# Kernel tuning notes

Measured on AMD Instinct MI355X. Metric: run time of the kernel, lower is better.

The kernel has to match this reference:

```python
import jax, jax.numpy as jnp
import numpy as np

# ReRAM crossbar constants (from init_kwargs)
GMAX = 0.000333
GMIN = 3.33e-07
DELTA_G = GMAX - GMIN
VDD = 3.3
N_LVL_V = 256
DELTA_V = VDD / (N_LVL_V - 1)
CRXB_COL, CRXB_ROW, CRXB_SIZE = 16, 16, 64
BATCH = 4096


def setup_inputs() -> dict:
    key = jax.random.key(0)
    k1, k2 = jax.random.split(key)
    inputs = jax.random.normal(k1, (BATCH, 1, CRXB_ROW, CRXB_SIZE, 1), dtype=jnp.float32)
    weight = jax.random.normal(k2, (CRXB_COL, CRXB_ROW, CRXB_SIZE, CRXB_SIZE), dtype=jnp.float32)
    nchout_index = jnp.arange(CRXB_COL * CRXB_SIZE, dtype=jnp.int64)
    return {"inputs": inputs, "weight": weight, "nchout_index": nchout_index}


def reference(inputs, weight, nchout_index):
    # DAC: scale digital input to voltage
    input_crxb = inputs * DELTA_V                      # [N,1,row,S,1]
    # w2g: map signed weight to positive/negative conductance crossbars
    g_pos = GMIN + jax.nn.relu(weight) * DELTA_G       # [col,row,S,S]
    g_neg = GMIN + jax.nn.relu(-weight) * DELTA_G
    # split pos/neg crossbar matmuls (broadcast over batch), fused subtract
    out = jnp.matmul(g_pos, input_crxb) - jnp.matmul(g_neg, input_crxb)  # [N,col,row,S,1]
    out = jnp.swapaxes(out, 2, 3)                      # [N,col,S,row,1]
    n = out.shape[0]
    out = out.reshape(n, CRXB_COL * CRXB_SIZE, CRXB_ROW, 1)
    out = jnp.take(out, nchout_index, axis=1)          # output channel select
    return jnp.squeeze(out, axis=-1)                   # [N, col*S, row]
```

## Files before the change

### kernel.cpp

```cpp
#include <hip/hip_runtime.h>
#include <hip/hip_bf16.h>
#include <stdint.h>


using bf16x8 = __attribute__((ext_vector_type(8))) short;
using f32x4  = __attribute__((ext_vector_type(4))) float;

#define NPT 16
#define NIT 16
#define PITCH_B 2064
#define BUFB 33024
#define LDS_BYTES (2*BUFB)

__device__ inline ushort f2bf(float f) {
  uint32_t u = __builtin_bit_cast(uint32_t, f);
  u += 0x7FFFu + ((u >> 16) & 1u);
  return (ushort)(u >> 16);
}

__device__ inline bf16x8 cvt8v(float4 a, float4 b) {
  union { bf16x8 v; ushort u[8]; } r;
  r.u[0] = f2bf(a.x); r.u[1] = f2bf(a.y); r.u[2] = f2bf(a.z); r.u[3] = f2bf(a.w);
  r.u[4] = f2bf(b.x); r.u[5] = f2bf(b.y); r.u[6] = f2bf(b.z); r.u[7] = f2bf(b.w);
  return r.v;
}

__global__ __launch_bounds__(512, 4)
void crxb_kernel(const float* __restrict__ X, const float* __restrict__ W,
                 float* __restrict__ out) {
  extern __shared__ char smem[];
  const int t   = threadIdx.x;
  const int bid = blockIdx.x;
  const int ngrp = ((bid & 7) << 1) | ((bid >> 3) & 1);
  const int mt   = bid >> 4;
  const int c  = mt >> 1;
  const int i0 = (mt & 1) << 5;
  const int m0 = mt << 5;

  const int wid = t >> 6;
  const int l   = t & 63;
  const int lr  = l & 15;
  const int lk  = l >> 4;
  const int r0w = wid << 1;

  bf16x8 A[2][2][2];
  #pragma unroll
  for (int rr = 0; rr < 2; ++rr)
    #pragma unroll
    for (int ks = 0; ks < 2; ++ks)
      #pragma unroll
      for (int a = 0; a < 2; ++a) {
        const float* gw = W + (((size_t)(c * 16 + r0w + rr) * 64) + (i0 + a * 16 + lr)) * 64
                            + ks * 32 + lk * 8;
        A[rr][ks][a] = cvt8v(*(const float4*)gw, *(const float4*)(gw + 4));
      }

  const float S = (float)((0.000333 - 3.33e-07) * (3.3 / 255.0));

  {
    #pragma unroll
    for (int p = 0; p < 4; ++p) {
      int u = p * 512 + t;
      int n = u >> 7, r = (u >> 3) & 15, k8 = u & 7;
      const float* gx = X + (((size_t)(ngrp * 256 + n) * 16) + r) * 64 + k8 * 8;
      *(bf16x8*)(smem + (size_t)n * PITCH_B + r * 128 + k8 * 16) =
          cvt8v(*(const float4*)gx, *(const float4*)(gx + 4));
    }
  }
  __syncthreads();

  int cur = 0;
  for (int it = 0; it < NIT; ++it) {
    char* bufc = smem + cur * BUFB;
    char* bufn = smem + (cur ^ 1) * BUFB;
    const int n0 = ngrp * 256 + it * NPT;

    float4 xp[8];
    if (it + 1 < NIT) {
      #pragma unroll
      for (int p = 0; p < 4; ++p) {
        int u = p * 512 + t;
        int n = u >> 7, r = (u >> 3) & 15, k8 = u & 7;
        const float* gx = X + (((size_t)(n0 + NPT + n) * 16) + r) * 64 + k8 * 8;
        xp[2 * p]     = *(const float4*)gx;
        xp[2 * p + 1] = *(const float4*)(gx + 4);
      }
    }

    f32x4 acc[2][2];
    #pragma unroll
    for (int rr = 0; rr < 2; ++rr)
      #pragma unroll
      for (int a = 0; a < 2; ++a) acc[rr][a] = (f32x4){0.f, 0.f, 0.f, 0.f};

    #pragma unroll
    for (int rr = 0; rr < 2; ++rr) {
      const int r = r0w + rr;
      #pragma unroll
      for (int ks = 0; ks < 2; ++ks) {
        bf16x8 Bf = *(const bf16x8*)(bufc + (size_t)lr * PITCH_B + r * 128 + ks * 64 + lk * 16);
        acc[rr][0] = __builtin_amdgcn_mfma_f32_16x16x32_bf16(A[rr][ks][0], Bf, acc[rr][0], 0, 0, 0);
        acc[rr][1] = __builtin_amdgcn_mfma_f32_16x16x32_bf16(A[rr][ks][1], Bf, acc[rr][1], 0, 0, 0);
      }
    }
    __syncthreads();

    #pragma unroll
    for (int a = 0; a < 2; ++a)
      #pragma unroll
      for (int reg = 0; reg < 4; ++reg) {
        float2 v = make_float2(acc[0][a][reg] * S, acc[1][a][reg] * S);
        *(float2*)(bufc + ((size_t)lr * 516 + a * 256 + lk * 64 + reg * 16 + r0w) * 4) = v;
      }
    __syncthreads();

    {
      const int n  = t >> 5;
      const int j0 = t & 31;
      float* gout = out + ((size_t)(n0 + n)) * 16384 + (size_t)m0 * 16;
      const float* Or = (const float*)(bufc + (size_t)n * PITCH_B);
      #pragma unroll
      for (int q = 0; q < 4; ++q)
        *(float4*)(gout + (q * 32 + j0) * 4) = *(const float4*)(Or + (q * 32 + j0) * 4);
    }

    if (it + 1 < NIT) {
      #pragma unroll
      for (int p = 0; p < 4; ++p) {
        int u = p * 512 + t;
        int n = u >> 7, r = (u >> 3) & 15, k8 = u & 7;
        *(bf16x8*)(bufn + (size_t)n * PITCH_B + r * 128 + k8 * 16) = cvt8v(xp[2 * p], xp[2 * p + 1]);
      }
    }
    __syncthreads();
    cur ^= 1;
  }
}

extern "C" void kernel_launch(void* const* d_in, const int* in_sizes, int n_in,
                              void* d_out, int out_size, void* d_ws, size_t ws_size,
                              hipStream_t stream) {
  const float* X = (const float*)d_in[0];
  const float* W = (const float*)d_in[1];
  float* out = (float*)d_out;
  (void)in_sizes; (void)n_in; (void)d_ws; (void)ws_size; (void)out_size;

  hipFuncSetAttribute(reinterpret_cast<const void*>(crxb_kernel),
                      hipFuncAttributeMaxDynamicSharedMemorySize, LDS_BYTES);

  crxb_kernel<<<dim3(512), dim3(512), LDS_BYTES, stream>>>(X, W, out);
}
```

Before: 61.54 us.

## Load X directly from global into MFMA operands, drop LDS double buffering

The input tile is no longer staged as bf16 in a double-buffered LDS region. Each lane now loads its X fragment straight from global memory and converts it in registers before the MFMA. The grid doubles to 1024 blocks, each handling 128 batch rows instead of 256, and occupancy is raised to 6 blocks per CU thanks to the smaller LDS footprint. The output staging changes to a 514-float pitch with nontemporal float2 stores. The redundant per-wave global reads of X rely on cache hits and lose the explicit prefetch overlap. The doubled grid also repeats the weight conversion work in twice as many blocks.

```diff
diff --git a/kernel.cpp b/kernel.cpp
--- a/kernel.cpp
+++ b/kernel.cpp
@@ -1,16 +1,13 @@
 #include <hip/hip_runtime.h>
-#include <hip/hip_bf16.h>
 #include <stdint.h>
 
 
 using bf16x8 = __attribute__((ext_vector_type(8))) short;
 using f32x4  = __attribute__((ext_vector_type(4))) float;
+using f32x2  = __attribute__((ext_vector_type(2))) float;
 
-#define NPT 16
-#define NIT 16
-#define PITCH_B 2064
-#define BUFB 33024
-#define LDS_BYTES (2*BUFB)
+#define PITCH_DW 514
+#define LDS_BYTES (16 * PITCH_DW * 4)
 
 __device__ inline ushort f2bf(float f) {
   uint32_t u = __builtin_bit_cast(uint32_t, f);
@@ -25,14 +22,18 @@
   return r.v;
 }
 
-__global__ __launch_bounds__(512, 4)
+__global__ __launch_bounds__(512, 6)
 void crxb_kernel(const float* __restrict__ X, const float* __restrict__ W,
                  float* __restrict__ out) {
   extern __shared__ char smem[];
+  float* O = (float*)smem;
+
   const int t   = threadIdx.x;
   const int bid = blockIdx.x;
-  const int ngrp = ((bid & 7) << 1) | ((bid >> 3) & 1);
-  const int mt   = bid >> 4;
+  const int xcd  = bid & 7;
+  const int slot = bid >> 3;
+  const int ng   = xcd * 4 + (slot & 3);
+  const int mt   = slot >> 2;
   const int c  = mt >> 1;
   const int i0 = (mt & 1) << 5;
   const int m0 = mt << 5;
@@ -57,35 +58,8 @@
 
   const float S = (float)((0.000333 - 3.33e-07) * (3.3 / 255.0));
 
-  {
-    #pragma unroll
-    for (int p = 0; p < 4; ++p) {
-      int u = p * 512 + t;
-      int n = u >> 7, r = (u >> 3) & 15, k8 = u & 7;
-      const float* gx = X + (((size_t)(ngrp * 256 + n) * 16) + r) * 64 + k8 * 8;
-      *(bf16x8*)(smem + (size_t)n * PITCH_B + r * 128 + k8 * 16) =
-          cvt8v(*(const float4*)gx, *(const float4*)(gx + 4));
-    }
-  }
-  __syncthreads();
-
-  int cur = 0;
-  for (int it = 0; it < NIT; ++it) {
-    char* bufc = smem + cur * BUFB;
-    char* bufn = smem + (cur ^ 1) * BUFB;
-    const int n0 = ngrp * 256 + it * NPT;
-
-    float4 xp[8];
-    if (it + 1 < NIT) {
-      #pragma unroll
-      for (int p = 0; p < 4; ++p) {
-        int u = p * 512 + t;
-        int n = u >> 7, r = (u >> 3) & 15, k8 = u & 7;
-        const float* gx = X + (((size_t)(n0 + NPT + n) * 16) + r) * 64 + k8 * 8;
-        xp[2 * p]     = *(const float4*)gx;
-        xp[2 * p + 1] = *(const float4*)(gx + 4);
-      }
-    }
+  for (int it = 0; it < 8; ++it) {
+    const int n0 = ng * 128 + it * 16;
 
     f32x4 acc[2][2];
     #pragma unroll
@@ -95,45 +69,41 @@
 
     #pragma unroll
     for (int rr = 0; rr < 2; ++rr) {
-      const int r = r0w + rr;
+      const float* xb = X + (size_t)(n0 + lr) * 1024 + (r0w + rr) * 64;
       #pragma unroll
       for (int ks = 0; ks < 2; ++ks) {
-        bf16x8 Bf = *(const bf16x8*)(bufc + (size_t)lr * PITCH_B + r * 128 + ks * 64 + lk * 16);
+        float4 xa = *(const float4*)(xb + ks * 32 + lk * 8);
+        float4 xc = *(const float4*)(xb + ks * 32 + lk * 8 + 4);
+        bf16x8 Bf = cvt8v(xa, xc);
         acc[rr][0] = __builtin_amdgcn_mfma_f32_16x16x32_bf16(A[rr][ks][0], Bf, acc[rr][0], 0, 0, 0);
         acc[rr][1] = __builtin_amdgcn_mfma_f32_16x16x32_bf16(A[rr][ks][1], Bf, acc[rr][1], 0, 0, 0);
       }
     }
+
     __syncthreads();
 
     #pragma unroll
     for (int a = 0; a < 2; ++a)
       #pragma unroll
       for (int reg = 0; reg < 4; ++reg) {
-        float2 v = make_float2(acc[0][a][reg] * S, acc[1][a][reg] * S);
-        *(float2*)(bufc + ((size_t)lr * 516 + a * 256 + lk * 64 + reg * 16 + r0w) * 4) = v;
+        f32x2 v = {acc[0][a][reg] * S, acc[1][a][reg] * S};
+        const int mm = a * 16 + lk * 4 + reg;
+        *(f32x2*)(O + (size_t)lr * PITCH_DW + mm * 16 + r0w) = v;
       }
     __syncthreads();
 
     {
       const int n  = t >> 5;
       const int j0 = t & 31;
+      const float* Or = O + (size_t)n * PITCH_DW;
       float* gout = out + ((size_t)(n0 + n)) * 16384 + (size_t)m0 * 16;
-      const float* Or = (const float*)(bufc + (size_t)n * PITCH_B);
       #pragma unroll
-      for (int q = 0; q < 4; ++q)
-        *(float4*)(gout + (q * 32 + j0) * 4) = *(const float4*)(Or + (q * 32 + j0) * 4);
-    }
-
-    if (it + 1 < NIT) {
-      #pragma unroll
-      for (int p = 0; p < 4; ++p) {
-        int u = p * 512 + t;
-        int n = u >> 7, r = (u >> 3) & 15, k8 = u & 7;
-        *(bf16x8*)(bufn + (size_t)n * PITCH_B + r * 128 + k8 * 16) = cvt8v(xp[2 * p], xp[2 * p + 1]);
+      for (int q = 0; q < 8; ++q) {
+        const int u = (q * 32 + j0) * 2;
+        f32x2 v = *(const f32x2*)(Or + u);
+        __builtin_nontemporal_store(v, (f32x2*)(gout + u));
       }
     }
-    __syncthreads();
-    cur ^= 1;
   }
 }
 
@@ -148,5 +118,5 @@
   hipFuncSetAttribute(reinterpret_cast<const void*>(crxb_kernel),
                       hipFuncAttributeMaxDynamicSharedMemorySize, LDS_BYTES);
 
-  crxb_kernel<<<dim3(512), dim3(512), LDS_BYTES, stream>>>(X, W, out);
+  crxb_kernel<<<dim3(1024), dim3(512), LDS_BYTES, stream>>>(X, W, out);
 }
```

After: 91.96 us. +49.4%, slower.

## Double grid size, relax barriers, and use nontemporal output stores

Applied to the files above, without the earlier changes.

Launches 1024 blocks with half the batch range per block and remaps block IDs so each XCD covers a contiguous set of batch groups. Replaces __syncthreads with an inline LDS-only wait plus s_barrier so global prefetch loads are not drained at each barrier. Output stores become nontemporal to reduce cache pollution on the large write stream. The extra blocks re-load and convert weights more often, and the custom barrier relies on the compiler inserting vmcnt waits before the prefetched registers are used.

```diff
diff --git a/kernel.cpp b/kernel.cpp
--- a/kernel.cpp
+++ b/kernel.cpp
@@ -1,16 +1,18 @@
 #include <hip/hip_runtime.h>
-#include <hip/hip_bf16.h>
 #include <stdint.h>
 
 
 using bf16x8 = __attribute__((ext_vector_type(8))) short;
 using f32x4  = __attribute__((ext_vector_type(4))) float;
+using f32x2  = __attribute__((ext_vector_type(2))) float;
 
 #define NPT 16
-#define NIT 16
+#define NIT 8
 #define PITCH_B 2064
 #define BUFB 33024
 #define LDS_BYTES (2*BUFB)
+
+#define BARRIER() asm volatile("s_waitcnt lgkmcnt(0)\n\ts_barrier" ::: "memory")
 
 __device__ inline ushort f2bf(float f) {
   uint32_t u = __builtin_bit_cast(uint32_t, f);
@@ -31,8 +33,9 @@
   extern __shared__ char smem[];
   const int t   = threadIdx.x;
   const int bid = blockIdx.x;
-  const int ngrp = ((bid & 7) << 1) | ((bid >> 3) & 1);
-  const int mt   = bid >> 4;
+  const int xcd  = bid & 7;
+  const int ng   = xcd * 4 + ((bid >> 3) & 3);
+  const int mt   = bid >> 5;
   const int c  = mt >> 1;
   const int i0 = (mt & 1) << 5;
   const int m0 = mt << 5;
@@ -62,18 +65,18 @@
     for (int p = 0; p < 4; ++p) {
       int u = p * 512 + t;
       int n = u >> 7, r = (u >> 3) & 15, k8 = u & 7;
-      const float* gx = X + (((size_t)(ngrp * 256 + n) * 16) + r) * 64 + k8 * 8;
+      const float* gx = X + (((size_t)(ng * 128 + n) * 16) + r) * 64 + k8 * 8;
       *(bf16x8*)(smem + (size_t)n * PITCH_B + r * 128 + k8 * 16) =
           cvt8v(*(const float4*)gx, *(const float4*)(gx + 4));
     }
   }
-  __syncthreads();
+  BARRIER();
 
   int cur = 0;
   for (int it = 0; it < NIT; ++it) {
     char* bufc = smem + cur * BUFB;
     char* bufn = smem + (cur ^ 1) * BUFB;
-    const int n0 = ngrp * 256 + it * NPT;
+    const int n0 = ng * 128 + it * NPT;
 
     float4 xp[8];
     if (it + 1 < NIT) {
@@ -103,25 +106,29 @@
         acc[rr][1] = __builtin_amdgcn_mfma_f32_16x16x32_bf16(A[rr][ks][1], Bf, acc[rr][1], 0, 0, 0);
       }
     }
-    __syncthreads();
+    BARRIER();
 
     #pragma unroll
     for (int a = 0; a < 2; ++a)
       #pragma unroll
       for (int reg = 0; reg < 4; ++reg) {
-        float2 v = make_float2(acc[0][a][reg] * S, acc[1][a][reg] * S);
-        *(float2*)(bufc + ((size_t)lr * 516 + a * 256 + lk * 64 + reg * 16 + r0w) * 4) = v;
+        f32x2 v = {acc[0][a][reg] * S, acc[1][a][reg] * S};
+        const int mm = a * 16 + lk * 4 + reg;
+        *(f32x2*)(bufc + ((size_t)lr * 516 + mm * 16 + r0w) * 4) = v;
       }
-    __syncthreads();
+    BARRIER();
 
     {
       const int n  = t >> 5;
       const int j0 = t & 31;
+      const float* Or = (const float*)(bufc + (size_t)n * PITCH_B);
       float* gout = out + ((size_t)(n0 + n)) * 16384 + (size_t)m0 * 16;
-      const float* Or = (const float*)(bufc + (size_t)n * PITCH_B);
       #pragma unroll
-      for (int q = 0; q < 4; ++q)
-        *(float4*)(gout + (q * 32 + j0) * 4) = *(const float4*)(Or + (q * 32 + j0) * 4);
+      for (int q = 0; q < 4; ++q) {
+        const int u = (q * 32 + j0) * 4;
+        f32x4 v = *(const f32x4*)(Or + u);
+        __builtin_nontemporal_store(v, (f32x4*)(gout + u));
+      }
     }
 
     if (it + 1 < NIT) {
@@ -132,7 +139,7 @@
         *(bf16x8*)(bufn + (size_t)n * PITCH_B + r * 128 + k8 * 16) = cvt8v(xp[2 * p], xp[2 * p + 1]);
       }
     }
-    __syncthreads();
+    BARRIER();
     cur ^= 1;
   }
 }
@@ -145,8 +152,8 @@
   float* out = (float*)d_out;
   (void)in_sizes; (void)n_in; (void)d_ws; (void)ws_size; (void)out_size;
 
-  hipFuncSetAttribute(reinterpret_cast<const void*>(crxb_kernel),
-                      hipFuncAttributeMaxDynamicSharedMemorySize, LDS_BYTES);
+  (void)hipFuncSetAttribute(reinterpret_cast<const void*>(crxb_kernel),
+                            hipFuncAttributeMaxDynamicSharedMemorySize, LDS_BYTES);
 
-  crxb_kernel<<<dim3(512), dim3(512), LDS_BYTES, stream>>>(X, W, out);
+  crxb_kernel<<<dim3(1024), dim3(512), LDS_BYTES, stream>>>(X, W, out);
 }
```

Result: slower. 72.54 us (+17.9%).
